# Performance work log

Hardware: AMD Instinct MI355X
Metric: run time of the kernel (lower is better)

Reference implementation:

```python
import jax, jax.numpy as jnp
import numpy as np
from jax.scipy.special import ndtr

TOKENS, D, E, K = 8192, 4096, 16, 4  # tokens, input_size, num_experts, num_selects
NOISE_EPS = 0.01
BALANCE_W = 0.01


def setup_inputs() -> dict:
    key = jax.random.key(0)
    k1, k2, k3, k4, k5 = jax.random.split(key, 5)
    x = jax.random.normal(k1, (TOKENS, D), dtype=jnp.float32)
    noise = jax.random.normal(k2, (TOKENS, E), dtype=jnp.float32)  # randn_like(logits)
    # mlp gate: Linear(D,E,bias=False) -> Tanh -> Linear(E,E,bias=False); default torch init scale
    Wg1 = jax.random.normal(k3, (E, D), dtype=jnp.float32) / np.sqrt(D)
    Wg2 = jax.random.normal(k4, (E, E), dtype=jnp.float32) / np.sqrt(E)
    # weight_noise is zero-initialized in the module, but use small random values
    # so the noise path is exercised
    Wn = jax.random.normal(k5, (E, D), dtype=jnp.float32) * 0.02
    return {"x": x, "noise": noise, "Wg1": Wg1, "Wg2": Wg2, "Wn": Wn}


def reference(x, noise, Wg1, Wg2, Wn):
    # gate logits: mlp gate network
    h = jnp.tanh(x @ Wg1.T)                      # [N, E]
    logits_gate = h @ Wg2.T                      # [N, E]
    # noisy logits (training + add_noise path)
    noise_control = jax.nn.softplus(x @ Wn.T) + NOISE_EPS  # [N, E]
    logits_noise = noise * noise_control
    logits = logits_gate + logits_noise
    # top-(k+1), torch.topk is sorted descending like lax.top_k
    m = min(K + 1, E)
    top_logits, top_indices = jax.lax.top_k(logits, m)     # [N, m]
    top_k_logits = top_logits[:, :K]
    top_k_indices = top_indices[:, :K]
    top_k_scores = jax.nn.softmax(top_k_logits, axis=1)    # use_softmax
    # importance: scatter top-k scores back to [N, E] and sum over tokens
    N = x.shape[0]
    rows = jnp.arange(N)[:, None]
    scores_filtered = jnp.zeros_like(logits).at[rows, top_k_indices].set(top_k_scores)
    importance = scores_filtered.sum(0)                    # [E]
    # load: smooth estimator via normal CDF
    threshold_if_in = top_logits[:, K:K + 1]               # (k+1)-th value, [N,1]
    threshold_if_out = top_logits[:, K - 1:K]              # k-th value, [N,1]
    is_in = logits_noise > threshold_if_in
    prob_if_in = ndtr((logits_gate - threshold_if_in) / noise_control)
    prob_if_out = ndtr((logits_gate - threshold_if_out) / noise_control)
    prob = jnp.where(is_in, prob_if_in, prob_if_out)
    load = prob.sum(0)                                     # [E]
    # balance loss: cv^2 with unbiased variance (torch default)
    def cv_squared(v, eps=1e-10):
        return jnp.var(v, ddof=1) / (jnp.mean(v) ** 2 + eps)
    balance_loss = (cv_squared(importance) + cv_squared(load)) * BALANCE_W
    return top_k_scores, balance_loss, load, importance, top_k_indices
```

## Files before the change

kernel.cpp:

```cpp
#include <hip/hip_runtime.h>
#include <math.h>

#define TOKENS 8192
#define DDIM   4096
#define NE     16
#define NOUT   32
#define BKA    32
#define BMA    128
#define XSTR   134

#define OUT_BAL  32768
#define OUT_LOAD 32769
#define OUT_IMP  32785
#define OUT_IDX  32801

__global__ __launch_bounds__(256, 2) void gate_gemm_partial(
    const float* __restrict__ x,
    const float* __restrict__ Wg1,
    const float* __restrict__ Wn,
    float* __restrict__ P,
    int kchunk)
{
    __shared__ float xs[BKA * XSTR];

    const int tid = threadIdx.x;
    const int t0  = blockIdx.x * BMA;
    const int kc  = blockIdx.y * kchunk;
    const int tg  = tid & 63;
    const int og  = __builtin_amdgcn_readfirstlane(tid >> 6);

    const float* wrow[8];
#pragma unroll
    for (int j = 0; j < 8; ++j) {
        const int o = og * 8 + j;
        wrow[j] = (o < NE) ? (Wg1 + (size_t)o * DDIM)
                           : (Wn  + (size_t)(o - NE) * DDIM);
    }

    float acc[2][8];
#pragma unroll
    for (int i = 0; i < 2; ++i)
#pragma unroll
        for (int j = 0; j < 8; ++j) acc[i][j] = 0.0f;

    const int ns = kchunk / BKA;
    for (int s = 0; s < ns; ++s) {
        const int kb = kc + s * BKA;
#pragma unroll
        for (int p = 0; p < 4; ++p) {
            const int i2 = p * 256 + tid;
            const int ti = i2 >> 3;
            const int kf = i2 & 7;
            const float4 v = *(const float4*)(x + (size_t)(t0 + ti) * DDIM + kb + kf * 4);
            xs[(kf * 4 + 0) * XSTR + ti] = v.x;
            xs[(kf * 4 + 1) * XSTR + ti] = v.y;
            xs[(kf * 4 + 2) * XSTR + ti] = v.z;
            xs[(kf * 4 + 3) * XSTR + ti] = v.w;
        }
        __syncthreads();
#pragma unroll 4
        for (int k = 0; k < BKA; ++k) {
            const float2 xv = *(const float2*)&xs[k * XSTR + 2 * tg];
#pragma unroll
            for (int j = 0; j < 8; ++j) {
                const float w = wrow[j][kb + k];
                acc[0][j] = fmaf(xv.x, w, acc[0][j]);
                acc[1][j] = fmaf(xv.y, w, acc[1][j]);
            }
        }
        __syncthreads();
    }

    const size_t cb = (size_t)blockIdx.y * TOKENS * NOUT;
#pragma unroll
    for (int i = 0; i < 2; ++i) {
        const int t = t0 + 2 * tg + i;
        float4 a; a.x = acc[i][0]; a.y = acc[i][1]; a.z = acc[i][2]; a.w = acc[i][3];
        float4 b; b.x = acc[i][4]; b.y = acc[i][5]; b.z = acc[i][6]; b.w = acc[i][7];
        *(float4*)(P + cb + (size_t)t * NOUT + og * 8)     = a;
        *(float4*)(P + cb + (size_t)t * NOUT + og * 8 + 4) = b;
    }
}

__global__ __launch_bounds__(256) void gate_epilogue(
    const float* __restrict__ P,
    const float* __restrict__ noise,
    const float* __restrict__ Wg2,
    float* __restrict__ out,
    float* __restrict__ gacc,
    int nkc)
{
    __shared__ float s_imp[NE];
    __shared__ float s_load[NE];

    const int tid = threadIdx.x;
    if (tid < NE) { s_imp[tid] = 0.0f; s_load[tid] = 0.0f; }
    __syncthreads();

    const int t     = blockIdx.x * 16 + (tid >> 4);
    const int e     = tid & 15;
    const int lane  = tid & 63;
    const int gbase = lane & 48;

    float g1 = 0.0f, nn = 0.0f;
    for (int c = 0; c < nkc; ++c) {
        const float* pr = P + (size_t)c * TOKENS * NOUT + (size_t)t * NOUT;
        g1 += pr[e];
        nn += pr[NE + e];
    }

    float w2r[16];
#pragma unroll
    for (int r = 0; r < 4; ++r) {
        const float4 w = *(const float4*)(Wg2 + e * NE + r * 4);
        w2r[r * 4 + 0] = w.x; w2r[r * 4 + 1] = w.y;
        w2r[r * 4 + 2] = w.z; w2r[r * 4 + 3] = w.w;
    }

    const float h = tanhf(g1);
    float gate = 0.0f;
#pragma unroll
    for (int j = 0; j < 16; ++j) {
        const float hj = __shfl(h, gbase + j, 64);
        gate = fmaf(w2r[j], hj, gate);
    }

    const float nv  = noise[(size_t)t * NE + e];
    const float sp  = fmaxf(nn, 0.0f) + log1pf(expf(-fabsf(nn)));
    const float ncv = sp + 0.01f;
    const float ln  = nv * ncv;
    const float lg  = gate + ln;

    float tv[5]; int tix[5];
    bool masked = false;
#pragma unroll
    for (int r = 0; r < 5; ++r) {
        float cv = masked ? -INFINITY : lg;
        int   ci = e;
#pragma unroll
        for (int st = 1; st < 16; st <<= 1) {
            const float ov = __shfl_xor(cv, st, 64);
            const int   oi = __shfl_xor(ci, st, 64);
            const bool take = (ov > cv) || (ov == cv && oi < ci);
            cv = take ? ov : cv;
            ci = take ? oi : ci;
        }
        tv[r] = cv; tix[r] = ci;
        masked = masked || (e == ci);
    }

    const float m = tv[0];
    const float ssum = expf(tv[0] - m) + expf(tv[1] - m)
                     + expf(tv[2] - m) + expf(tv[3] - m);
    const float inv = 1.0f / ssum;

    if (e < 4) {
        const float myv = (e == 0) ? tv[0] : (e == 1) ? tv[1] : (e == 2) ? tv[2] : tv[3];
        const int   myi = (e == 0) ? tix[0] : (e == 1) ? tix[1] : (e == 2) ? tix[2] : tix[3];
        const float sc  = expf(myv - m) * inv;
        out[(size_t)t * 4 + e]           = sc;
        out[OUT_IDX + (size_t)t * 4 + e] = (float)myi;
        atomicAdd(&s_imp[myi], sc);
    }

    const float thr = (ln > tv[4]) ? tv[4] : tv[3];
    const float pr  = 0.5f * erfcf((thr - gate) * 0.70710678118654752440f / ncv);
    atomicAdd(&s_load[e], pr);
    __syncthreads();

    if (tid < NE)          atomicAdd(gacc + tid, s_imp[tid]);
    else if (tid < 2 * NE) atomicAdd(gacc + tid, s_load[tid - NE]);
}

__global__ void gate_finalize(const float* __restrict__ gacc, float* __restrict__ out)
{
    const int tid = threadIdx.x;
    if (tid == 0) {
        double mi = 0.0, ml = 0.0;
        for (int e = 0; e < NE; ++e) { mi += gacc[e]; ml += gacc[NE + e]; }
        mi /= NE; ml /= NE;
        double vi = 0.0, vl = 0.0;
        for (int e = 0; e < NE; ++e) {
            const double di = gacc[e] - mi;      vi += di * di;
            const double dl = gacc[NE + e] - ml; vl += dl * dl;
        }
        vi /= (NE - 1); vl /= (NE - 1);
        const double cvi = vi / (mi * mi + 1e-10);
        const double cvl = vl / (ml * ml + 1e-10);
        out[OUT_BAL] = (float)(0.01 * (cvi + cvl));
    }
    if (tid < NE) {
        out[OUT_LOAD + tid] = gacc[NE + tid];
        out[OUT_IMP  + tid] = gacc[tid];
    }
}

extern "C" void kernel_launch(void* const* d_in, const int* in_sizes, int n_in,
                              void* d_out, int out_size, void* d_ws, size_t ws_size,
                              hipStream_t stream)
{
    const float* x     = (const float*)d_in[0];
    const float* noise = (const float*)d_in[1];
    const float* Wg1   = (const float*)d_in[2];
    const float* Wg2   = (const float*)d_in[3];
    const float* Wn    = (const float*)d_in[4];
    float* out = (float*)d_out;

    float* gacc = (float*)d_ws;
    float* P    = gacc + 64;

    int nkc = 16;
    while (nkc > 1 && 256 + (size_t)nkc * TOKENS * NOUT * sizeof(float) > ws_size)
        nkc >>= 1;
    const int kchunk = DDIM / nkc;

    hipMemsetAsync(gacc, 0, 32 * sizeof(float), stream);

    dim3 gA(TOKENS / BMA, nkc);
    gate_gemm_partial<<<gA, 256, 0, stream>>>(x, Wg1, Wn, P, kchunk);
    gate_epilogue<<<TOKENS / 16, 256, 0, stream>>>(P, noise, Wg2, out, gacc, nkc);
    gate_finalize<<<1, 64, 0, stream>>>(gacc, out);
}
```

Measured before the change: 237.7 us.

## Rewrite gate GEMM as per-wave register-resident split-K with shuffle reduction

Replaces the LDS-tiled gate GEMM with a kernel in which each wavefront handles 8 tokens by 8 k-lanes. Each lane keeps all 32 output accumulators and the weight float4s in registers, and prefetches x and W one slab ahead. Partial sums are reduced across k-lanes with butterfly shuffles, and the P layout becomes token-major so the epilogue reads each token's split-K partials contiguously. This removes LDS staging and __syncthreads. In exchange it raises register pressure (32 acc plus 32 float4 weights), which can lower occupancy or cause spills, and each lane issues many uncoalesced global weight loads.

After: 350.5 us. +47.5%, slower.

```diff
diff --git a/kernel.cpp b/kernel.cpp
--- a/kernel.cpp
+++ b/kernel.cpp
@@ -5,81 +5,104 @@
 #define DDIM   4096
 #define NE     16
 #define NOUT   32
-#define BKA    32
-#define BMA    128
-#define XSTR   134
 
 #define OUT_BAL  32768
 #define OUT_LOAD 32769
 #define OUT_IMP  32785
 #define OUT_IDX  32801
 
-__global__ __launch_bounds__(256, 2) void gate_gemm_partial(
+__global__ __launch_bounds__(256, 2) void gate_gemm(
     const float* __restrict__ x,
     const float* __restrict__ Wg1,
     const float* __restrict__ Wn,
     float* __restrict__ P,
-    int kchunk)
-{
-    __shared__ float xs[BKA * XSTR];
-
-    const int tid = threadIdx.x;
-    const int t0  = blockIdx.x * BMA;
-    const int kc  = blockIdx.y * kchunk;
-    const int tg  = tid & 63;
-    const int og  = __builtin_amdgcn_readfirstlane(tid >> 6);
-
-    const float* wrow[8];
-#pragma unroll
-    for (int j = 0; j < 8; ++j) {
-        const int o = og * 8 + j;
-        wrow[j] = (o < NE) ? (Wg1 + (size_t)o * DDIM)
-                           : (Wn  + (size_t)(o - NE) * DDIM);
-    }
-
-    float acc[2][8];
-#pragma unroll
-    for (int i = 0; i < 2; ++i)
-#pragma unroll
-        for (int j = 0; j < 8; ++j) acc[i][j] = 0.0f;
-
-    const int ns = kchunk / BKA;
-    for (int s = 0; s < ns; ++s) {
-        const int kb = kc + s * BKA;
-#pragma unroll
-        for (int p = 0; p < 4; ++p) {
-            const int i2 = p * 256 + tid;
-            const int ti = i2 >> 3;
-            const int kf = i2 & 7;
-            const float4 v = *(const float4*)(x + (size_t)(t0 + ti) * DDIM + kb + kf * 4);
-            xs[(kf * 4 + 0) * XSTR + ti] = v.x;
-            xs[(kf * 4 + 1) * XSTR + ti] = v.y;
-            xs[(kf * 4 + 2) * XSTR + ti] = v.z;
-            xs[(kf * 4 + 3) * XSTR + ti] = v.w;
-        }
-        __syncthreads();
-#pragma unroll 4
-        for (int k = 0; k < BKA; ++k) {
-            const float2 xv = *(const float2*)&xs[k * XSTR + 2 * tg];
-#pragma unroll
-            for (int j = 0; j < 8; ++j) {
-                const float w = wrow[j][kb + k];
-                acc[0][j] = fmaf(xv.x, w, acc[0][j]);
-                acc[1][j] = fmaf(xv.y, w, acc[1][j]);
+    int lcs, int nslab)
+{
+    const int tid  = threadIdx.x;
+    const int lane = tid & 63;
+    const int wid  = blockIdx.x * 4 + (tid >> 6);
+    const int cs   = 1 << lcs;
+    const int c    = wid & (cs - 1);
+    const int t8   = wid >> lcs;
+    const int kq   = lane & 7;
+    const int tau  = lane >> 3;
+    const int t    = t8 * 8 + tau;
+    const int kbase = c * (nslab * 32);
+
+    const float* xp = x + (size_t)t * DDIM + kbase + 4 * kq;
+
+    float acc[NOUT];
+#pragma unroll
+    for (int o = 0; o < NOUT; ++o) acc[o] = 0.0f;
+
+    float4 xq0 = *(const float4*)(xp + 0 * 32);
+    float4 xq1 = *(const float4*)(xp + 1 * 32);
+    float4 xq2 = *(const float4*)(xp + 2 * 32);
+    float4 xq3 = *(const float4*)(xp + 3 * 32);
+
+    float4 wq[NOUT];
+#pragma unroll
+    for (int o = 0; o < NOUT; ++o) {
+        const float* wr = (o < NE) ? (Wg1 + (size_t)o * DDIM)
+                                   : (Wn  + (size_t)(o - NE) * DDIM);
+        wq[o] = *(const float4*)(wr + kbase + 4 * kq);
+    }
+
+    const int ngroups = nslab >> 2;
+    for (int g = 0; g < ngroups; ++g) {
+        const int gn = (g + 1 < ngroups) ? g + 1 : g;
+        const float4 xn0 = *(const float4*)(xp + (gn * 4 + 0) * 32);
+        const float4 xn1 = *(const float4*)(xp + (gn * 4 + 1) * 32);
+        const float4 xn2 = *(const float4*)(xp + (gn * 4 + 2) * 32);
+        const float4 xn3 = *(const float4*)(xp + (gn * 4 + 3) * 32);
+
+#pragma unroll
+        for (int ss = 0; ss < 4; ++ss) {
+            const float4 xc = (ss == 0) ? xq0 : (ss == 1) ? xq1
+                            : (ss == 2) ? xq2 : xq3;
+            const int sidx = g * 4 + ss;
+            const int noff = kbase + 4 * kq
+                           + ((sidx + 1 < nslab) ? (sidx + 1) : sidx) * 32;
+#pragma unroll
+            for (int o = 0; o < NOUT; ++o) {
+                const float4 f = wq[o];
+                acc[o] = fmaf(f.x, xc.x, acc[o]);
+                acc[o] = fmaf(f.y, xc.y, acc[o]);
+                acc[o] = fmaf(f.z, xc.z, acc[o]);
+                acc[o] = fmaf(f.w, xc.w, acc[o]);
+                const float* wr = (o < NE) ? (Wg1 + (size_t)o * DDIM)
+                                           : (Wn  + (size_t)(o - NE) * DDIM);
+                wq[o] = *(const float4*)(wr + noff);
             }
         }
-        __syncthreads();
-    }
-
-    const size_t cb = (size_t)blockIdx.y * TOKENS * NOUT;
-#pragma unroll
-    for (int i = 0; i < 2; ++i) {
-        const int t = t0 + 2 * tg + i;
-        float4 a; a.x = acc[i][0]; a.y = acc[i][1]; a.z = acc[i][2]; a.w = acc[i][3];
-        float4 b; b.x = acc[i][4]; b.y = acc[i][5]; b.z = acc[i][6]; b.w = acc[i][7];
-        *(float4*)(P + cb + (size_t)t * NOUT + og * 8)     = a;
-        *(float4*)(P + cb + (size_t)t * NOUT + og * 8 + 4) = b;
-    }
+        xq0 = xn0; xq1 = xn1; xq2 = xn2; xq3 = xn3;
+    }
+
+    const int sel1 = kq & 1, sel2 = (kq >> 1) & 1, sel3 = kq >> 2;
+    float l1[16];
+#pragma unroll
+    for (int i = 0; i < 16; ++i) {
+        const float mine = sel1 ? acc[16 + i] : acc[i];
+        const float send = sel1 ? acc[i]      : acc[16 + i];
+        l1[i] = mine + __shfl_xor(send, 1, 64);
+    }
+    float l2[8];
+#pragma unroll
+    for (int i = 0; i < 8; ++i) {
+        const float mine = sel2 ? l1[8 + i] : l1[i];
+        const float send = sel2 ? l1[i]     : l1[8 + i];
+        l2[i] = mine + __shfl_xor(send, 2, 64);
+    }
+    float l3[4];
+#pragma unroll
+    for (int i = 0; i < 4; ++i) {
+        const float mine = sel3 ? l2[4 + i] : l2[i];
+        const float send = sel3 ? l2[i]     : l2[4 + i];
+        l3[i] = mine + __shfl_xor(send, 4, 64);
+    }
+    const int obase = sel1 * 16 + sel2 * 8 + sel3 * 4;
+    float4 r; r.x = l3[0]; r.y = l3[1]; r.z = l3[2]; r.w = l3[3];
+    *(float4*)(P + ((size_t)t * cs + c) * NOUT + obase) = r;
 }
 
 __global__ __launch_bounds__(256) void gate_epilogue(
@@ -88,7 +111,7 @@
     const float* __restrict__ Wg2,
     float* __restrict__ out,
     float* __restrict__ gacc,
-    int nkc)
+    int cs)
 {
     __shared__ float s_imp[NE];
     __shared__ float s_load[NE];
@@ -102,11 +125,12 @@
     const int lane  = tid & 63;
     const int gbase = lane & 48;
 
+    const float* pr = P + (size_t)t * cs * NOUT;
     float g1 = 0.0f, nn = 0.0f;
-    for (int c = 0; c < nkc; ++c) {
-        const float* pr = P + (size_t)c * TOKENS * NOUT + (size_t)t * NOUT;
-        g1 += pr[e];
-        nn += pr[NE + e];
+#pragma unroll 8
+    for (int c = 0; c < cs; ++c) {
+        g1 += pr[c * NOUT + e];
+        nn += pr[c * NOUT + NE + e];
     }
 
     float w2r[16];
@@ -164,8 +188,8 @@
     }
 
     const float thr = (ln > tv[4]) ? tv[4] : tv[3];
-    const float pr  = 0.5f * erfcf((thr - gate) * 0.70710678118654752440f / ncv);
-    atomicAdd(&s_load[e], pr);
+    const float pr2 = 0.5f * erfcf((thr - gate) * 0.70710678118654752440f / ncv);
+    atomicAdd(&s_load[e], pr2);
     __syncthreads();
 
     if (tid < NE)          atomicAdd(gacc + tid, s_imp[tid]);
@@ -209,15 +233,16 @@
     float* gacc = (float*)d_ws;
     float* P    = gacc + 64;
 
-    int nkc = 16;
-    while (nkc > 1 && 256 + (size_t)nkc * TOKENS * NOUT * sizeof(float) > ws_size)
-        nkc >>= 1;
-    const int kchunk = DDIM / nkc;
+    int cs = 16, lcs = 4;
+    while (cs > 1 && 256 + (size_t)cs * TOKENS * NOUT * sizeof(float) > ws_size) {
+        cs >>= 1; lcs -= 1;
+    }
+    const int nslab = DDIM / (cs * 32);
 
     hipMemsetAsync(gacc, 0, 32 * sizeof(float), stream);
 
-    dim3 gA(TOKENS / BMA, nkc);
-    gate_gemm_partial<<<gA, 256, 0, stream>>>(x, Wg1, Wn, P, kchunk);
-    gate_epilogue<<<TOKENS / 16, 256, 0, stream>>>(P, noise, Wg2, out, gacc, nkc);
+    const int nblocks = (TOKENS / 8) * cs / 4;
+    gate_gemm<<<nblocks, 256, 0, stream>>>(x, Wg1, Wn, P, lcs, nslab);
+    gate_epilogue<<<TOKENS / 16, 256, 0, stream>>>(P, noise, Wg2, out, gacc, cs);
     gate_finalize<<<1, 64, 0, stream>>>(gacc, out);
 }
```
